# Kernel optimization log

Hardware: AMD Instinct MI355X
Metric: run time of the kernel (lower is better)

Reference implementation:

```python
import jax, jax.numpy as jnp
import numpy as np

H = 16
D_MODEL = 1024
D_K = D_MODEL // H
B, S = 2, 2048


def setup_inputs() -> dict:
    key = jax.random.key(0)
    ks = jax.random.split(key, 11)
    scale = 1.0 / np.sqrt(D_MODEL)
    inp = {
        "query": jax.random.normal(ks[0], (B, S, D_MODEL), jnp.float32),
        "key": jax.random.normal(ks[1], (B, S, D_MODEL), jnp.float32),
        "value": jax.random.normal(ks[2], (B, S, D_MODEL), jnp.float32),
        # four nn.Linear(d_model, d_model): Wq, Wk, Wv, Wo (torch convention: y = x @ W.T + b)
        "Wq": jax.random.uniform(ks[3], (D_MODEL, D_MODEL), jnp.float32, -scale, scale),
        "bq": jax.random.uniform(ks[4], (D_MODEL,), jnp.float32, -scale, scale),
        "Wk": jax.random.uniform(ks[5], (D_MODEL, D_MODEL), jnp.float32, -scale, scale),
        "bk": jax.random.uniform(ks[6], (D_MODEL,), jnp.float32, -scale, scale),
        "Wv": jax.random.uniform(ks[7], (D_MODEL, D_MODEL), jnp.float32, -scale, scale),
        "bv": jax.random.uniform(ks[8], (D_MODEL,), jnp.float32, -scale, scale),
        "Wo": jax.random.uniform(ks[9], (D_MODEL, D_MODEL), jnp.float32, -scale, scale),
        "bo": jax.random.uniform(ks[10], (D_MODEL,), jnp.float32, -scale, scale),
    }
    return inp


def _split_heads(x):
    # [B, S, D] -> [B, H, S, d_k]
    b, s, _ = x.shape
    return x.reshape(b, s, H, D_K).transpose(0, 2, 1, 3)


def reference(query, key, value, Wq, bq, Wk, bk, Wv, bv, Wo, bo):
    q = _split_heads(query @ Wq.T + bq)
    k = _split_heads(key @ Wk.T + bk)
    v = _split_heads(value @ Wv.T + bv)
    # scaled dot-product attention (dropout omitted: reference is eval-mode)
    scores = jnp.einsum("bhqd,bhkd->bhqk", q, k) / np.sqrt(D_K).astype(np.float32)
    p = jax.nn.softmax(scores, axis=-1)
    x = jnp.einsum("bhqk,bhkd->bhqd", p, v)
    x = x.transpose(0, 2, 1, 3).reshape(query.shape[0], -1, H * D_K)
    return x @ Wo.T + bo
```

## Files before the change

### kernel.cpp

```cpp
#include <hip/hip_runtime.h>

typedef unsigned short u16;
typedef unsigned int u32;
typedef __attribute__((ext_vector_type(8))) short short8;
typedef __attribute__((ext_vector_type(8))) _Float16 half8;
typedef __attribute__((ext_vector_type(4))) float floatx4;
typedef __attribute__((ext_vector_type(4))) unsigned short ushortx4;
typedef __attribute__((ext_vector_type(4))) unsigned int uint4v;

#define DEV static __device__ __forceinline__

DEV float bf2f(u16 u) { union { unsigned u; float f; } v; v.u = ((unsigned)u) << 16; return v.f; }
DEV u16 f2bf(float f) {
  union { float f; unsigned u; } v; v.f = f;
  return (u16)((v.u + 0x7FFFu + ((v.u >> 16) & 1u)) >> 16);
}
DEV u16 f2h(float f) { return __builtin_bit_cast(u16, (_Float16)f); }
DEV u32 pkh(float a, float b) {
  return __builtin_bit_cast(u32, __builtin_amdgcn_cvt_pkrtz(a, b));
}
DEV float fexp2(float x) { return __builtin_amdgcn_exp2f(x); }

#define GLDS(g, l) __builtin_amdgcn_global_load_lds( \
    (const __attribute__((address_space(1))) void*)(g), \
    (__attribute__((address_space(3))) void*)(l), 16, 0, 0)

struct CvtArg {
  const float* src[11];
  u16* dst[11];
  int cum[12];
};

__global__ void convert(CvtArg a) {
  const long base = ((long)blockIdx.x * 256 + threadIdx.x) * 4;
  if (base >= a.cum[11]) return;
  int s = 0;
  while (s < 10 && base >= a.cum[s + 1]) ++s;
  const long off = base - a.cum[s];
  const float* sp = a.src[s] + off;
  ushortx4 u;
#pragma unroll
  for (int r = 0; r < 4; ++r) u[r] = f2bf(sp[r]);
  *(ushortx4*)(a.dst[s] + off) = u;
}

struct GemmArg {
  const u16* x;
  const u16* w;
  const u16* bias;
  u16* dst;
  int mode;
};

__global__ __launch_bounds__(256, 2) void gemm_nt(GemmArg g0, GemmArg g1, GemmArg g2) {
  GemmArg g = (blockIdx.z == 0) ? g0 : ((blockIdx.z == 1) ? g1 : g2);
  __shared__ u16 As[128 * 32];
  __shared__ u16 Bs[128 * 32];
  const int tid = threadIdx.x, w = tid >> 6, l = tid & 63;
  const int l15 = l & 15, quad = l >> 4;
  const int bm = blockIdx.x, bn = blockIdx.y;
  const int wm = w >> 1, wn = w & 1;

  floatx4 acc[4][4];
#pragma unroll
  for (int i = 0; i < 4; ++i)
#pragma unroll
    for (int j = 0; j < 4; ++j) acc[i][j] = (floatx4){0.f, 0.f, 0.f, 0.f};

  const u16* xb = g.x + (long)(bm * 128 + w * 16 + (l >> 2)) * 1024 + (l & 3) * 8;
  const u16* wb = g.w + (long)(bn * 128 + w * 16 + (l >> 2)) * 1024 + (l & 3) * 8;
  u16* asb = &As[(w * 16) * 32];
  u16* bsb = &Bs[(w * 16) * 32];

  for (int kt = 0; kt < 32; ++kt) {
    const int k0 = kt * 32;
    __syncthreads();
#pragma unroll
    for (int p = 0; p < 2; ++p) {
      GLDS(xb + (long)p * 64 * 1024 + k0, asb + p * 64 * 32);
      GLDS(wb + (long)p * 64 * 1024 + k0, bsb + p * 64 * 32);
    }
    __syncthreads();
    short8 af[4], bfr[4];
#pragma unroll
    for (int mi = 0; mi < 4; ++mi)
      af[mi] = *(const short8*)&As[(wm * 64 + mi * 16 + l15) * 32 + quad * 8];
#pragma unroll
    for (int ni = 0; ni < 4; ++ni)
      bfr[ni] = *(const short8*)&Bs[(wn * 64 + ni * 16 + l15) * 32 + quad * 8];
#pragma unroll
    for (int mi = 0; mi < 4; ++mi)
#pragma unroll
      for (int ni = 0; ni < 4; ++ni)
        acc[mi][ni] = __builtin_amdgcn_mfma_f32_16x16x32_bf16(af[mi], bfr[ni], acc[mi][ni], 0, 0, 0);
  }

  float bv[4];
#pragma unroll
  for (int ni = 0; ni < 4; ++ni) bv[ni] = bf2f(g.bias[bn * 128 + wn * 64 + ni * 16 + l15]);

#pragma unroll
  for (int mi = 0; mi < 4; ++mi) {
    const int mbase = bm * 128 + wm * 64 + mi * 16 + quad * 4;
#pragma unroll
    for (int ni = 0; ni < 4; ++ni) {
      const int n = bn * 128 + wn * 64 + ni * 16 + l15;
      if (g.mode == 2) {
        const int b = mbase >> 11, s = mbase & 2047;
        const int h = n >> 6, d = n & 63;
        ushortx4 u;
#pragma unroll
        for (int r = 0; r < 4; ++r) u[r] = f2h(acc[mi][ni][r] + bv[ni]);
        *(ushortx4*)&g.dst[((long)(b * 16 + h) * 64 + d) * 2048 + s] = u;
      } else if (g.mode == 3) {
        float* df = (float*)g.dst;
#pragma unroll
        for (int r = 0; r < 4; ++r)
          df[(long)(mbase + r) * 1024 + n] = acc[mi][ni][r] + bv[ni];
      } else {
        const float sc = (g.mode == 0) ? 0.18033688011f : 1.0f;
        const int h = n >> 6, d = n & 63;
#pragma unroll
        for (int r = 0; r < 4; ++r) {
          const int m = mbase + r, b = m >> 11, s = m & 2047;
          g.dst[((long)(b * 16 + h) * 2048 + s) * 64 + d] = f2bf((acc[mi][ni][r] + bv[ni]) * sc);
        }
      }
    }
  }
}

__global__ __launch_bounds__(256, 2) void attn_flash(const u16* __restrict__ Q,
                                                     const u16* __restrict__ K,
                                                     const u16* __restrict__ V,
                                                     u16* __restrict__ X) {
  __shared__ u16 KVs[4][64 * 72];
  const int tid = threadIdx.x, w = tid >> 6, l = tid & 63;
  const int l15 = l & 15, quad = l >> 4;
  const int qh = w >> 1, kh = w & 1;

  const int bid = blockIdx.x;
  const int xcd = bid & 7, idx = bid >> 3;
  const int qx = idx & 15, bh = xcd + 8 * (idx >> 4);
  const int q0 = qx * 128;

  const u16* qp = Q + (long)bh * 2048 * 64;
  const u16* kp = K + (long)bh * 2048 * 64;
  const u16* vp = V + (long)bh * 2048 * 64;

  const int r0 = tid >> 3, c0 = tid & 7, r1 = 32 + (tid >> 3);

#define ISSUE_LOADS(kv0) \
    sk0 = *(const short8*)(kp + (long)((kv0) + r0) * 64 + c0 * 8); \
    sv0 = *(const short8*)(vp + (long)r0 * 2048 + (kv0) + c0 * 8); \
    sk1 = *(const short8*)(kp + (long)((kv0) + r1) * 64 + c0 * 8); \
    sv1 = *(const short8*)(vp + (long)r1 * 2048 + (kv0) + c0 * 8);

#define STORE_TILE(pb_) \
    *(short8*)&KVs[pb_][r0 * 72 + c0 * 8] = sk0; \
    *(short8*)&KVs[2 + (pb_)][r0 * 72 + c0 * 8] = sv0; \
    *(short8*)&KVs[pb_][r1 * 72 + c0 * 8] = sk1; \
    *(short8*)&KVs[2 + (pb_)][r1 * 72 + c0 * 8] = sv1;

  short8 sk0, sv0, sk1, sv1;

  short8 qf[4][2];
#pragma unroll
  for (int nq = 0; nq < 4; ++nq)
#pragma unroll
    for (int kc = 0; kc < 2; ++kc)
      qf[nq][kc] = *(const short8*)(qp + (long)(q0 + qh * 64 + nq * 16 + l15) * 64 + kc * 32 + quad * 8);

  floatx4 o[4][4];
#pragma unroll
  for (int nq = 0; nq < 4; ++nq)
#pragma unroll
    for (int nd = 0; nd < 4; ++nd) o[nq][nd] = (floatx4){0.f, 0.f, 0.f, 0.f};
  float den[4] = {0.f, 0.f, 0.f, 0.f};

  const bool p1 = (l & 32) != 0;
  const bool p3 = (l & 16) != 0;
  const bool p2 = p1 ^ p3;

#define BFLY(pbv, m00, m01, m10, m11) { \
    u32 A0 = p1 ? (m10) : (m00), A1 = p1 ? (m11) : (m01); \
    u32 s0_ = p1 ? (m00) : (m10), s1_ = p1 ? (m01) : (m11); \
    u32 B0 = (u32)__shfl_xor((int)s0_, 32), B1 = (u32)__shfl_xor((int)s1_, 32); \
    u32 t0 = p2 ? A0 : B0, t1 = p2 ? A1 : B1; \
    u32 u0 = (u32)__shfl_xor((int)t0, 16), u1 = (u32)__shfl_xor((int)t1, 16); \
    u32 w0 = p2 ? B0 : A0, w1 = p2 ? B1 : A1; \
    pbv[0] = p3 ? u0 : w0; pbv[1] = p3 ? u1 : w1; \
    pbv[2] = p3 ? w0 : u0; pbv[3] = p3 ? w1 : u1; \
  }

  ISSUE_LOADS(0)
  STORE_TILE(0)
  ISSUE_LOADS(64)
  __syncthreads();

  for (int t = 0; t < 32; ++t) {
    const int p = t & 1;

    u32 pk[4][2][2];
#pragma unroll
    for (int mk = 0; mk < 2; ++mk) {
      const int krow = kh * 32 + mk * 16 + l15;
      short8 ak0 = *(const short8*)&KVs[p][krow * 72 + quad * 8];
      short8 ak1 = *(const short8*)&KVs[p][krow * 72 + 32 + quad * 8];
#pragma unroll
      for (int nq = 0; nq < 4; ++nq) {
        floatx4 st = (floatx4){0.f, 0.f, 0.f, 0.f};
        st = __builtin_amdgcn_mfma_f32_16x16x32_bf16(ak0, qf[nq][0], st, 0, 0, 0);
        st = __builtin_amdgcn_mfma_f32_16x16x32_bf16(ak1, qf[nq][1], st, 0, 0, 0);
        const float e0 = fexp2(st[0]), e1 = fexp2(st[1]);
        const float e2 = fexp2(st[2]), e3 = fexp2(st[3]);
        den[nq] += (e0 + e1) + (e2 + e3);
        pk[nq][mk][0] = pkh(e0, e1);
        pk[nq][mk][1] = pkh(e2, e3);
      }
    }

    half8 vf[4];
#pragma unroll
    for (int nd = 0; nd < 4; ++nd)
      vf[nd] = *(const half8*)&KVs[2 + p][(nd * 16 + l15) * 72 + kh * 32 + quad * 8];
#pragma unroll
    for (int nq = 0; nq < 4; ++nq) {
      uint4v pb;
      BFLY(pb, pk[nq][0][0], pk[nq][0][1], pk[nq][1][0], pk[nq][1][1])
      half8 pbs = __builtin_bit_cast(half8, pb);
#pragma unroll
      for (int nd = 0; nd < 4; ++nd)
        o[nq][nd] = __builtin_amdgcn_mfma_f32_16x16x32_f16(vf[nd], pbs, o[nq][nd], 0, 0, 0);
    }

    if (t < 31) {
      STORE_TILE(p ^ 1)
      if (t < 30) {
        ISSUE_LOADS((t + 2) * 64)
      }
    }
    __syncthreads();
  }

  float dsum[4];
#pragma unroll
  for (int nq = 0; nq < 4; ++nq) {
    float d = den[nq];
    d += __shfl_xor(d, 16);
    d += __shfl_xor(d, 32);
    dsum[nq] = d;
  }

  float* osc = (float*)KVs;
  float* dsc = osc + 8192;
  if (kh == 1) {
#pragma unroll
    for (int nq = 0; nq < 4; ++nq)
#pragma unroll
      for (int nd = 0; nd < 4; ++nd)
        *(floatx4*)&osc[(((qh * 4 + nq) * 4 + nd) * 64 + l) * 4] = o[nq][nd];
    if (l < 16) {
#pragma unroll
      for (int nq = 0; nq < 4; ++nq) dsc[(qh * 4 + nq) * 16 + l] = dsum[nq];
    }
  }
  __syncthreads();

  if (kh == 0) {
    float rcp[4];
#pragma unroll
    for (int nq = 0; nq < 4; ++nq) rcp[nq] = 1.0f / (dsum[nq] + dsc[(qh * 4 + nq) * 16 + l15]);
    const int b = bh >> 4, h = bh & 15;
#pragma unroll
    for (int nq = 0; nq < 4; ++nq) {
      const int s = q0 + qh * 64 + nq * 16 + l15;
      u16* xrow = X + ((long)(b * 2048 + s)) * 1024 + h * 64;
#pragma unroll
      for (int nd = 0; nd < 4; ++nd) {
        floatx4 om = o[nq][nd] + *(const floatx4*)&osc[(((qh * 4 + nq) * 4 + nd) * 64 + l) * 4];
        ushortx4 u;
#pragma unroll
        for (int r = 0; r < 4; ++r) u[r] = f2bf(om[r] * rcp[nq]);
        *(ushortx4*)&xrow[nd * 16 + quad * 4] = u;
      }
    }
  }
}

extern "C" void kernel_launch(void* const* d_in, const int* in_sizes, int n_in,
                              void* d_out, int out_size, void* d_ws, size_t ws_size,
                              hipStream_t stream) {
  u16* ws = (u16*)d_ws;
  const size_t M1 = 1048576, M4 = 4194304;
  u16* NQ  = ws;
  u16* NK  = ws + M4;
  u16* NV  = ws + 2 * M4;
  u16* NWQ = ws + 3 * M4;
  u16* NWK = ws + 3 * M4 + M1;
  u16* NWV = ws + 3 * M4 + 2 * M1;
  u16* NWO = ws + 3 * M4 + 3 * M1;
  u16* NBQ = ws + 3 * M4 + 4 * M1;
  u16* NBK = NBQ + 1024;
  u16* NBV = NBQ + 2048;
  u16* NBO = NBQ + 3072;
  u16* Qb = ws + 16 * M1 + 8192;
  u16* Kb = Qb + M4;
  u16* Vb = Qb + 2 * M4;
  u16* Xb = NQ;

  CvtArg ca;
  u16* dsts[11] = {NQ, NK, NV, NWQ, NBQ, NWK, NBK, NWV, NBV, NWO, NBO};
  int sizes[11] = {(int)M4, (int)M4, (int)M4, (int)M1, 1024, (int)M1, 1024, (int)M1, 1024, (int)M1, 1024};
  int c = 0;
  for (int i = 0; i < 11; ++i) {
    ca.src[i] = (const float*)d_in[i];
    ca.dst[i] = dsts[i];
    ca.cum[i] = c;
    c += sizes[i];
  }
  ca.cum[11] = c;
  convert<<<(c / 4 + 255) / 256, 256, 0, stream>>>(ca);

  GemmArg gq{NQ, NWQ, NBQ, Qb, 0};
  GemmArg gk{NK, NWK, NBK, Kb, 1};
  GemmArg gv{NV, NWV, NBV, Vb, 2};
  gemm_nt<<<dim3(32, 8, 3), 256, 0, stream>>>(gq, gk, gv);

  attn_flash<<<dim3(512), 256, 0, stream>>>(Qb, Kb, Vb, Xb);

  GemmArg go{Xb, NWO, NBO, (u16*)d_out, 3};
  gemm_nt<<<dim3(32, 8, 1), 256, 0, stream>>>(go, go, go);
}
```

Measured before the change: 228.4 us.

## Double-buffer K/V prefetch registers and unroll attention loop by two

Splits the K/V prefetch registers into two alternating sets and unrolls the key loop by two. Each iteration now issues global loads two tiles ahead before storing the previously fetched tile into the other LDS buffer. Global load latency therefore gets a full iteration to resolve instead of a partial one. It also hoists all K and V LDS fragment reads to the top of the iteration so they overlap with the MFMAs, at the cost of more live VGPRs, which could lower occupancy or cause spills.

```diff
diff --git a/kernel.cpp b/kernel.cpp
--- a/kernel.cpp
+++ b/kernel.cpp
@@ -150,19 +150,31 @@
 
   const int r0 = tid >> 3, c0 = tid & 7, r1 = 32 + (tid >> 3);
 
-#define ISSUE_LOADS(kv0) \
-    sk0 = *(const short8*)(kp + (long)((kv0) + r0) * 64 + c0 * 8); \
-    sv0 = *(const short8*)(vp + (long)r0 * 2048 + (kv0) + c0 * 8); \
-    sk1 = *(const short8*)(kp + (long)((kv0) + r1) * 64 + c0 * 8); \
-    sv1 = *(const short8*)(vp + (long)r1 * 2048 + (kv0) + c0 * 8);
-
-#define STORE_TILE(pb_) \
-    *(short8*)&KVs[pb_][r0 * 72 + c0 * 8] = sk0; \
-    *(short8*)&KVs[2 + (pb_)][r0 * 72 + c0 * 8] = sv0; \
-    *(short8*)&KVs[pb_][r1 * 72 + c0 * 8] = sk1; \
-    *(short8*)&KVs[2 + (pb_)][r1 * 72 + c0 * 8] = sv1;
-
-  short8 sk0, sv0, sk1, sv1;
+  short8 skA0, svA0, skA1, svA1, skB0, svB0, skB1, svB1;
+
+#define ISSUE_LOADS_A(kv0) \
+    skA0 = *(const short8*)(kp + (long)((kv0) + r0) * 64 + c0 * 8); \
+    svA0 = *(const short8*)(vp + (long)r0 * 2048 + (kv0) + c0 * 8); \
+    skA1 = *(const short8*)(kp + (long)((kv0) + r1) * 64 + c0 * 8); \
+    svA1 = *(const short8*)(vp + (long)r1 * 2048 + (kv0) + c0 * 8);
+
+#define ISSUE_LOADS_B(kv0) \
+    skB0 = *(const short8*)(kp + (long)((kv0) + r0) * 64 + c0 * 8); \
+    svB0 = *(const short8*)(vp + (long)r0 * 2048 + (kv0) + c0 * 8); \
+    skB1 = *(const short8*)(kp + (long)((kv0) + r1) * 64 + c0 * 8); \
+    svB1 = *(const short8*)(vp + (long)r1 * 2048 + (kv0) + c0 * 8);
+
+#define STORE_TILE_A(pb_) \
+    *(short8*)&KVs[pb_][r0 * 72 + c0 * 8] = skA0; \
+    *(short8*)&KVs[2 + (pb_)][r0 * 72 + c0 * 8] = svA0; \
+    *(short8*)&KVs[pb_][r1 * 72 + c0 * 8] = skA1; \
+    *(short8*)&KVs[2 + (pb_)][r1 * 72 + c0 * 8] = svA1;
+
+#define STORE_TILE_B(pb_) \
+    *(short8*)&KVs[pb_][r0 * 72 + c0 * 8] = skB0; \
+    *(short8*)&KVs[2 + (pb_)][r0 * 72 + c0 * 8] = svB0; \
+    *(short8*)&KVs[pb_][r1 * 72 + c0 * 8] = skB1; \
+    *(short8*)&KVs[2 + (pb_)][r1 * 72 + c0 * 8] = svB1;
 
   short8 qf[4][2];
 #pragma unroll
@@ -193,54 +205,54 @@
     pbv[2] = p3 ? w0 : u0; pbv[3] = p3 ? w1 : u1; \
   }
 
-  ISSUE_LOADS(0)
-  STORE_TILE(0)
-  ISSUE_LOADS(64)
+#define ATTN_ITER(t, p, IS, ST) { \
+    if ((t) < 30) { IS(((t) + 2) * 64) } \
+    if ((t) < 31) { ST((p) ^ 1) } \
+    const int kr0 = kh * 32 + l15, kr1 = kh * 32 + 16 + l15; \
+    short8 ak00 = *(const short8*)&KVs[p][kr0 * 72 + quad * 8]; \
+    short8 ak01 = *(const short8*)&KVs[p][kr0 * 72 + 32 + quad * 8]; \
+    short8 ak10 = *(const short8*)&KVs[p][kr1 * 72 + quad * 8]; \
+    short8 ak11 = *(const short8*)&KVs[p][kr1 * 72 + 32 + quad * 8]; \
+    half8 vf0 = *(const half8*)&KVs[2 + (p)][(0 * 16 + l15) * 72 + kh * 32 + quad * 8]; \
+    half8 vf1 = *(const half8*)&KVs[2 + (p)][(1 * 16 + l15) * 72 + kh * 32 + quad * 8]; \
+    half8 vf2 = *(const half8*)&KVs[2 + (p)][(2 * 16 + l15) * 72 + kh * 32 + quad * 8]; \
+    half8 vf3 = *(const half8*)&KVs[2 + (p)][(3 * 16 + l15) * 72 + kh * 32 + quad * 8]; \
+    u32 pk[4][2][2]; \
+    _Pragma("unroll") \
+    for (int nq = 0; nq < 4; ++nq) { \
+      floatx4 st0 = (floatx4){0.f, 0.f, 0.f, 0.f}, st1 = (floatx4){0.f, 0.f, 0.f, 0.f}; \
+      st0 = __builtin_amdgcn_mfma_f32_16x16x32_bf16(ak00, qf[nq][0], st0, 0, 0, 0); \
+      st0 = __builtin_amdgcn_mfma_f32_16x16x32_bf16(ak01, qf[nq][1], st0, 0, 0, 0); \
+      st1 = __builtin_amdgcn_mfma_f32_16x16x32_bf16(ak10, qf[nq][0], st1, 0, 0, 0); \
+      st1 = __builtin_amdgcn_mfma_f32_16x16x32_bf16(ak11, qf[nq][1], st1, 0, 0, 0); \
+      float e0 = fexp2(st0[0]), e1 = fexp2(st0[1]), e2 = fexp2(st0[2]), e3 = fexp2(st0[3]); \
+      den[nq] += (e0 + e1) + (e2 + e3); \
+      pk[nq][0][0] = pkh(e0, e1); pk[nq][0][1] = pkh(e2, e3); \
+      e0 = fexp2(st1[0]); e1 = fexp2(st1[1]); e2 = fexp2(st1[2]); e3 = fexp2(st1[3]); \
+      den[nq] += (e0 + e1) + (e2 + e3); \
+      pk[nq][1][0] = pkh(e0, e1); pk[nq][1][1] = pkh(e2, e3); \
+    } \
+    _Pragma("unroll") \
+    for (int nq = 0; nq < 4; ++nq) { \
+      uint4v pb; \
+      BFLY(pb, pk[nq][0][0], pk[nq][0][1], pk[nq][1][0], pk[nq][1][1]) \
+      half8 pbs = __builtin_bit_cast(half8, pb); \
+      o[nq][0] = __builtin_amdgcn_mfma_f32_16x16x32_f16(vf0, pbs, o[nq][0], 0, 0, 0); \
+      o[nq][1] = __builtin_amdgcn_mfma_f32_16x16x32_f16(vf1, pbs, o[nq][1], 0, 0, 0); \
+      o[nq][2] = __builtin_amdgcn_mfma_f32_16x16x32_f16(vf2, pbs, o[nq][2], 0, 0, 0); \
+      o[nq][3] = __builtin_amdgcn_mfma_f32_16x16x32_f16(vf3, pbs, o[nq][3], 0, 0, 0); \
+    } \
+    __syncthreads(); \
+  }
+
+  ISSUE_LOADS_A(0)
+  STORE_TILE_A(0)
+  ISSUE_LOADS_B(64)
   __syncthreads();
 
-  for (int t = 0; t < 32; ++t) {
-    const int p = t & 1;
-
-    u32 pk[4][2][2];
-#pragma unroll
-    for (int mk = 0; mk < 2; ++mk) {
-      const int krow = kh * 32 + mk * 16 + l15;
-      short8 ak0 = *(const short8*)&KVs[p][krow * 72 + quad * 8];
-      short8 ak1 = *(const short8*)&KVs[p][krow * 72 + 32 + quad * 8];
-#pragma unroll
-      for (int nq = 0; nq < 4; ++nq) {
-        floatx4 st = (floatx4){0.f, 0.f, 0.f, 0.f};
-        st = __builtin_amdgcn_mfma_f32_16x16x32_bf16(ak0, qf[nq][0], st, 0, 0, 0);
-        st = __builtin_amdgcn_mfma_f32_16x16x32_bf16(ak1, qf[nq][1], st, 0, 0, 0);
-        const float e0 = fexp2(st[0]), e1 = fexp2(st[1]);
-        const float e2 = fexp2(st[2]), e3 = fexp2(st[3]);
-        den[nq] += (e0 + e1) + (e2 + e3);
-        pk[nq][mk][0] = pkh(e0, e1);
-        pk[nq][mk][1] = pkh(e2, e3);
-      }
-    }
-
-    half8 vf[4];
-#pragma unroll
-    for (int nd = 0; nd < 4; ++nd)
-      vf[nd] = *(const half8*)&KVs[2 + p][(nd * 16 + l15) * 72 + kh * 32 + quad * 8];
-#pragma unroll
-    for (int nq = 0; nq < 4; ++nq) {
-      uint4v pb;
-      BFLY(pb, pk[nq][0][0], pk[nq][0][1], pk[nq][1][0], pk[nq][1][1])
-      half8 pbs = __builtin_bit_cast(half8, pb);
-#pragma unroll
-      for (int nd = 0; nd < 4; ++nd)
-        o[nq][nd] = __builtin_amdgcn_mfma_f32_16x16x32_f16(vf[nd], pbs, o[nq][nd], 0, 0, 0);
-    }
-
-    if (t < 31) {
-      STORE_TILE(p ^ 1)
-      if (t < 30) {
-        ISSUE_LOADS((t + 2) * 64)
-      }
-    }
-    __syncthreads();
+  for (int tt = 0; tt < 32; tt += 2) {
+    ATTN_ITER(tt, 0, ISSUE_LOADS_A, STORE_TILE_B)
+    ATTN_ITER(tt + 1, 1, ISSUE_LOADS_B, STORE_TILE_A)
   }
 
   float dsum[4];
```

Measured after the change: 227.9 us. Within noise of the previous version (-0.2%).
